# Kernel tuning notes

Hardware: AMD Instinct MI355X
Metric: run time of the kernel (lower is better)

The kernel has to match this reference:

```python
import jax, jax.numpy as jnp
import numpy as np

R, F, H = 256, 1024, 256  # num_robots, num_frontiers, hidden_dim


def setup_inputs() -> dict:
    key = jax.random.key(0)
    ks = jax.random.split(key, 16)
    sc = 0.05
    return {
        "robot_features": jax.random.normal(ks[0], (R, 4), jnp.float32),
        "frontier_features": jax.random.normal(ks[1], (F, 3), jnp.float32),
        # robot encoder: Linear(4,H) -> ReLU -> Linear(H,H)
        "r_w1": jax.random.normal(ks[2], (4, H), jnp.float32) * sc,
        "r_b1": jnp.zeros((H,), jnp.float32),
        "r_w2": jax.random.normal(ks[3], (H, H), jnp.float32) * sc,
        "r_b2": jnp.zeros((H,), jnp.float32),
        # frontier encoder: Linear(3,H) -> ReLU -> Linear(H,H)
        "f_w1": jax.random.normal(ks[4], (3, H), jnp.float32) * sc,
        "f_b1": jnp.zeros((H,), jnp.float32),
        "f_w2": jax.random.normal(ks[5], (H, H), jnp.float32) * sc,
        "f_b2": jnp.zeros((H,), jnp.float32),
        # affinity predictor: Linear(2H,H) -> ReLU -> Linear(H,1)
        "a_w1": jax.random.normal(ks[6], (2 * H, H), jnp.float32) * sc,
        "a_b1": jnp.zeros((H,), jnp.float32),
        "a_w2": jax.random.normal(ks[7], (H, 1), jnp.float32) * sc,
        "a_b2": jnp.zeros((1,), jnp.float32),
    }


def reference(robot_features, frontier_features,
              r_w1, r_b1, r_w2, r_b2,
              f_w1, f_b1, f_w2, f_b2,
              a_w1, a_b1, a_w2, a_b2):
    # encoders: Linear -> ReLU -> Linear
    robot_embed = jax.nn.relu(robot_features @ r_w1 + r_b1) @ r_w2 + r_b2      # (R, H)
    frontier_embed = jax.nn.relu(frontier_features @ f_w1 + f_b1) @ f_w2 + f_b2  # (F, H)

    # Vectorized pairwise concat: split a_w1 into robot/frontier halves so we
    # never materialize the (R, F, 2H) concat explicitly.
    w1_r, w1_f = a_w1[:robot_embed.shape[1]], a_w1[robot_embed.shape[1]:]
    h = robot_embed @ w1_r  # (R, H)
    h = h[:, None, :] + (frontier_embed @ w1_f)[None, :, :] + a_b1  # (R, F, H)
    h = jax.nn.relu(h)
    affinity = (h @ a_w2)[..., 0] + a_b2[0]  # (R, F)
    return affinity
```

## Files before the change

### kernel.cpp

```cpp
#include <hip/hip_runtime.h>
#include <hip/hip_bf16.h>

#define H 256
#define R_N 256
#define F_N 1024

#define FMA4(A, s, W) \
    A.x = fmaf((s), (W).x, A.x); \
    A.y = fmaf((s), (W).y, A.y); \
    A.z = fmaf((s), (W).z, A.z); \
    A.w = fmaf((s), (W).w, A.w);

__global__ __launch_bounds__(256) void embed_kernel(
    const float* __restrict__ rf, const float* __restrict__ ff,
    const float* __restrict__ r_w1, const float* __restrict__ r_b1,
    const float* __restrict__ r_w2, const float* __restrict__ r_b2,
    const float* __restrict__ f_w1, const float* __restrict__ f_b1,
    const float* __restrict__ f_w2, const float* __restrict__ f_b2,
    const float* __restrict__ a_w1, const float* __restrict__ a_b1,
    float* __restrict__ u, float* __restrict__ v)
{
    const int t  = threadIdx.x;
    const int wp = t >> 6;
    const int c  = (t & 63) * 4;

    __shared__ float aT[H][4];
    __shared__ float red[4][4][H];

    const bool robot = blockIdx.x < 64;
    const int  g0    = robot ? blockIdx.x * 4 : (blockIdx.x - 64) * 4;

    const float* __restrict__ x   = robot ? (rf + g0 * 4) : (ff + g0 * 3);
    const int                 ind = robot ? 4 : 3;
    const float* __restrict__ w1  = robot ? r_w1 : f_w1;
    const float* __restrict__ b1  = robot ? r_b1 : f_b1;
    const float* __restrict__ W2  = robot ? r_w2 : f_w2;
    const float* __restrict__ b2  = robot ? r_b2 : f_b2;
    const int                 k3  = robot ? 0 : H;
    float* __restrict__       dst = robot ? u : v;

    {
        float l1[4];
        const float bb = b1[t];
        #pragma unroll
        for (int g = 0; g < 4; ++g) {
            float acc = bb;
            for (int j = 0; j < ind; ++j)
                acc = fmaf(x[g * ind + j], w1[j * H + t], acc);
            l1[g] = fmaxf(acc, 0.0f);
        }
        *(float4*)&aT[t][0] = make_float4(l1[0], l1[1], l1[2], l1[3]);
    }
    __syncthreads();

    {
        float4 a0 = {0,0,0,0}, a1 = {0,0,0,0}, a2 = {0,0,0,0}, a3 = {0,0,0,0};
        const int kb = wp * 64;
        #pragma unroll 8
        for (int kk = 0; kk < 64; ++kk) {
            const int k = kb + kk;
            const float4 w4 = *(const float4*)&W2[k * H + c];
            const float4 av = *(const float4*)&aT[k][0];
            FMA4(a0, av.x, w4);
            FMA4(a1, av.y, w4);
            FMA4(a2, av.z, w4);
            FMA4(a3, av.w, w4);
        }
        *(float4*)&red[wp][0][c] = a0;
        *(float4*)&red[wp][1][c] = a1;
        *(float4*)&red[wp][2][c] = a2;
        *(float4*)&red[wp][3][c] = a3;
    }
    __syncthreads();

    {
        const float bb = b2[t];
        float e[4];
        #pragma unroll
        for (int g = 0; g < 4; ++g)
            e[g] = red[0][g][t] + red[1][g][t] + red[2][g][t] + red[3][g][t] + bb;
        __syncthreads();
        *(float4*)&aT[t][0] = make_float4(e[0], e[1], e[2], e[3]);
    }
    __syncthreads();

    {
        float4 a0 = {0,0,0,0}, a1 = {0,0,0,0}, a2 = {0,0,0,0}, a3 = {0,0,0,0};
        const int kb = wp * 64;
        #pragma unroll 8
        for (int kk = 0; kk < 64; ++kk) {
            const int k = kb + kk;
            const float4 w4 = *(const float4*)&a_w1[(k3 + k) * H + c];
            const float4 av = *(const float4*)&aT[k][0];
            FMA4(a0, av.x, w4);
            FMA4(a1, av.y, w4);
            FMA4(a2, av.z, w4);
            FMA4(a3, av.w, w4);
        }
        *(float4*)&red[wp][0][c] = a0;
        *(float4*)&red[wp][1][c] = a1;
        *(float4*)&red[wp][2][c] = a2;
        *(float4*)&red[wp][3][c] = a3;
    }
    __syncthreads();

    {
        const float ab = robot ? 0.0f : a_b1[t];
        #pragma unroll
        for (int g = 0; g < 4; ++g) {
            const float s = red[0][g][t] + red[1][g][t] + red[2][g][t] + red[3][g][t] + ab;
            dst[(g0 + g) * H + t] = s;
        }
    }
}

#define LDP 260

__global__ __launch_bounds__(512) void affinity_kernel(
    const float* __restrict__ u, const float* __restrict__ v,
    const float* __restrict__ a_w2, const float* __restrict__ a_b2,
    float* __restrict__ out)
{
    __shared__ float u_s[32][LDP];
    __shared__ float v_s[32][LDP];
    __shared__ float w_s[H];
    __shared__ float red[4][32][33];

    const int t  = threadIdx.x;
    const int r0 = (blockIdx.x >> 5) * 32;
    const int f0 = (blockIdx.x & 31) * 32;

    #pragma unroll
    for (int i = 0; i < 4; ++i) {
        const int slot = t + i * 512;
        const int row  = slot >> 6;
        const int cc   = (slot & 63) * 4;
        *(float4*)&u_s[row][cc] = *(const float4*)&u[(r0 + row) * H + cc];
        *(float4*)&v_s[row][cc] = *(const float4*)&v[(f0 + row) * H + cc];
    }
    if (t < 64) *(float4*)&w_s[t * 4] = *(const float4*)&a_w2[t * 4];
    __syncthreads();

    const int kp = t >> 7;
    const int t7 = t & 127;
    const int ri = t7 >> 4;
    const int fi = t7 & 15;
    const int k0 = kp * 64;

    float4 accA = make_float4(0.f, 0.f, 0.f, 0.f);
    float4 accB = make_float4(0.f, 0.f, 0.f, 0.f);

    #pragma unroll 4
    for (int kk = 0; kk < 64; kk += 4) {
        const int k = k0 + kk;
        const float4 w4 = *(const float4*)&w_s[k];
        const float4 u0 = *(const float4*)&u_s[ri][k];
        const float4 u1 = *(const float4*)&u_s[ri +  8][k];
        const float4 u2 = *(const float4*)&u_s[ri + 16][k];
        const float4 u3 = *(const float4*)&u_s[ri + 24][k];
        const float4 va = *(const float4*)&v_s[fi][k];
        const float4 vb = *(const float4*)&v_s[fi + 16][k];

        accA.x = fmaf(fmaxf(u0.x + va.x, 0.f), w4.x, accA.x);
        accA.x = fmaf(fmaxf(u0.y + va.y, 0.f), w4.y, accA.x);
        accA.x = fmaf(fmaxf(u0.z + va.z, 0.f), w4.z, accA.x);
        accA.x = fmaf(fmaxf(u0.w + va.w, 0.f), w4.w, accA.x);
        accA.y = fmaf(fmaxf(u1.x + va.x, 0.f), w4.x, accA.y);
        accA.y = fmaf(fmaxf(u1.y + va.y, 0.f), w4.y, accA.y);
        accA.y = fmaf(fmaxf(u1.z + va.z, 0.f), w4.z, accA.y);
        accA.y = fmaf(fmaxf(u1.w + va.w, 0.f), w4.w, accA.y);
        accA.z = fmaf(fmaxf(u2.x + va.x, 0.f), w4.x, accA.z);
        accA.z = fmaf(fmaxf(u2.y + va.y, 0.f), w4.y, accA.z);
        accA.z = fmaf(fmaxf(u2.z + va.z, 0.f), w4.z, accA.z);
        accA.z = fmaf(fmaxf(u2.w + va.w, 0.f), w4.w, accA.z);
        accA.w = fmaf(fmaxf(u3.x + va.x, 0.f), w4.x, accA.w);
        accA.w = fmaf(fmaxf(u3.y + va.y, 0.f), w4.y, accA.w);
        accA.w = fmaf(fmaxf(u3.z + va.z, 0.f), w4.z, accA.w);
        accA.w = fmaf(fmaxf(u3.w + va.w, 0.f), w4.w, accA.w);

        accB.x = fmaf(fmaxf(u0.x + vb.x, 0.f), w4.x, accB.x);
        accB.x = fmaf(fmaxf(u0.y + vb.y, 0.f), w4.y, accB.x);
        accB.x = fmaf(fmaxf(u0.z + vb.z, 0.f), w4.z, accB.x);
        accB.x = fmaf(fmaxf(u0.w + vb.w, 0.f), w4.w, accB.x);
        accB.y = fmaf(fmaxf(u1.x + vb.x, 0.f), w4.x, accB.y);
        accB.y = fmaf(fmaxf(u1.y + vb.y, 0.f), w4.y, accB.y);
        accB.y = fmaf(fmaxf(u1.z + vb.z, 0.f), w4.z, accB.y);
        accB.y = fmaf(fmaxf(u1.w + vb.w, 0.f), w4.w, accB.y);
        accB.z = fmaf(fmaxf(u2.x + vb.x, 0.f), w4.x, accB.z);
        accB.z = fmaf(fmaxf(u2.y + vb.y, 0.f), w4.y, accB.z);
        accB.z = fmaf(fmaxf(u2.z + vb.z, 0.f), w4.z, accB.z);
        accB.z = fmaf(fmaxf(u2.w + vb.w, 0.f), w4.w, accB.z);
        accB.w = fmaf(fmaxf(u3.x + vb.x, 0.f), w4.x, accB.w);
        accB.w = fmaf(fmaxf(u3.y + vb.y, 0.f), w4.y, accB.w);
        accB.w = fmaf(fmaxf(u3.z + vb.z, 0.f), w4.z, accB.w);
        accB.w = fmaf(fmaxf(u3.w + vb.w, 0.f), w4.w, accB.w);
    }

    red[kp][ri]     [fi]      = accA.x;
    red[kp][ri +  8][fi]      = accA.y;
    red[kp][ri + 16][fi]      = accA.z;
    red[kp][ri + 24][fi]      = accA.w;
    red[kp][ri]     [fi + 16] = accB.x;
    red[kp][ri +  8][fi + 16] = accB.y;
    red[kp][ri + 16][fi + 16] = accB.z;
    red[kp][ri + 24][fi + 16] = accB.w;
    __syncthreads();

    const float b = a_b2[0];
    #pragma unroll
    for (int j = 0; j < 2; ++j) {
        const int o = t + j * 512;
        const int r = o >> 5;
        const int f = o & 31;
        const float s = red[0][r][f] + red[1][r][f] + red[2][r][f] + red[3][r][f] + b;
        out[(r0 + r) * F_N + f0 + f] = s;
    }
}

extern "C" void kernel_launch(void* const* d_in, const int* in_sizes, int n_in,
                              void* d_out, int out_size, void* d_ws, size_t ws_size,
                              hipStream_t stream) {
    const float* rf   = (const float*)d_in[0];
    const float* ff   = (const float*)d_in[1];
    const float* r_w1 = (const float*)d_in[2];
    const float* r_b1 = (const float*)d_in[3];
    const float* r_w2 = (const float*)d_in[4];
    const float* r_b2 = (const float*)d_in[5];
    const float* f_w1 = (const float*)d_in[6];
    const float* f_b1 = (const float*)d_in[7];
    const float* f_w2 = (const float*)d_in[8];
    const float* f_b2 = (const float*)d_in[9];
    const float* a_w1 = (const float*)d_in[10];
    const float* a_b1 = (const float*)d_in[11];
    const float* a_w2 = (const float*)d_in[12];
    const float* a_b2 = (const float*)d_in[13];

    float* u = (float*)d_ws;
    float* v = u + R_N * H;

    embed_kernel<<<320, 256, 0, stream>>>(rf, ff, r_w1, r_b1, r_w2, r_b2,
                                          f_w1, f_b1, f_w2, f_b2,
                                          a_w1, a_b1, u, v);
    affinity_kernel<<<256, 512, 0, stream>>>(u, v, a_w2, a_b2, (float*)d_out);
}
```

Baseline: 26.11 us.

## Use 4x4 register tile per thread with 8-way K split in affinity kernel

Re-partitions the affinity kernel's thread work from a 4x2 (robot x frontier) output tile over a 4-way K split to a 4x4 tile over an 8-way K split of 32 columns each. Each thread loads 8 float4 rows from shared memory and reuses them for 16 accumulators instead of 6 loads for 8, cutting LDS traffic per FMA. In exchange the reduction buffer doubles to 8 partial slices and the final sum reads 8 values per output, adding shared memory and register pressure.

```diff
diff --git a/kernel.cpp b/kernel.cpp
--- a/kernel.cpp
+++ b/kernel.cpp
@@ -124,7 +124,7 @@
     __shared__ float u_s[32][LDP];
     __shared__ float v_s[32][LDP];
     __shared__ float w_s[H];
-    __shared__ float red[4][32][33];
+    __shared__ float red[8][32][33];
 
     const int t  = threadIdx.x;
     const int r0 = (blockIdx.x >> 5) * 32;
@@ -141,78 +141,58 @@
     if (t < 64) *(float4*)&w_s[t * 4] = *(const float4*)&a_w2[t * 4];
     __syncthreads();
 
-    const int kp = t >> 7;
-    const int t7 = t & 127;
-    const int ri = t7 >> 4;
-    const int fi = t7 & 15;
-    const int k0 = kp * 64;
-
-    float4 accA = make_float4(0.f, 0.f, 0.f, 0.f);
-    float4 accB = make_float4(0.f, 0.f, 0.f, 0.f);
+    const int kp = t >> 6;
+    const int t6 = t & 63;
+    const int ri = t6 & 7;
+    const int fi = t6 >> 3;
+    const int k0 = kp * 32;
+
+    float acc[4][4];
+    #pragma unroll
+    for (int a = 0; a < 4; ++a)
+        #pragma unroll
+        for (int b = 0; b < 4; ++b) acc[a][b] = 0.0f;
 
     #pragma unroll 4
-    for (int kk = 0; kk < 64; kk += 4) {
+    for (int kk = 0; kk < 32; kk += 4) {
         const int k = k0 + kk;
         const float4 w4 = *(const float4*)&w_s[k];
-        const float4 u0 = *(const float4*)&u_s[ri][k];
-        const float4 u1 = *(const float4*)&u_s[ri +  8][k];
-        const float4 u2 = *(const float4*)&u_s[ri + 16][k];
-        const float4 u3 = *(const float4*)&u_s[ri + 24][k];
-        const float4 va = *(const float4*)&v_s[fi][k];
-        const float4 vb = *(const float4*)&v_s[fi + 16][k];
-
-        accA.x = fmaf(fmaxf(u0.x + va.x, 0.f), w4.x, accA.x);
-        accA.x = fmaf(fmaxf(u0.y + va.y, 0.f), w4.y, accA.x);
-        accA.x = fmaf(fmaxf(u0.z + va.z, 0.f), w4.z, accA.x);
-        accA.x = fmaf(fmaxf(u0.w + va.w, 0.f), w4.w, accA.x);
-        accA.y = fmaf(fmaxf(u1.x + va.x, 0.f), w4.x, accA.y);
-        accA.y = fmaf(fmaxf(u1.y + va.y, 0.f), w4.y, accA.y);
-        accA.y = fmaf(fmaxf(u1.z + va.z, 0.f), w4.z, accA.y);
-        accA.y = fmaf(fmaxf(u1.w + va.w, 0.f), w4.w, accA.y);
-        accA.z = fmaf(fmaxf(u2.x + va.x, 0.f), w4.x, accA.z);
-        accA.z = fmaf(fmaxf(u2.y + va.y, 0.f), w4.y, accA.z);
-        accA.z = fmaf(fmaxf(u2.z + va.z, 0.f), w4.z, accA.z);
-        accA.z = fmaf(fmaxf(u2.w + va.w, 0.f), w4.w, accA.z);
-        accA.w = fmaf(fmaxf(u3.x + va.x, 0.f), w4.x, accA.w);
-        accA.w = fmaf(fmaxf(u3.y + va.y, 0.f), w4.y, accA.w);
-        accA.w = fmaf(fmaxf(u3.z + va.z, 0.f), w4.z, accA.w);
-        accA.w = fmaf(fmaxf(u3.w + va.w, 0.f), w4.w, accA.w);
-
-        accB.x = fmaf(fmaxf(u0.x + vb.x, 0.f), w4.x, accB.x);
-        accB.x = fmaf(fmaxf(u0.y + vb.y, 0.f), w4.y, accB.x);
-        accB.x = fmaf(fmaxf(u0.z + vb.z, 0.f), w4.z, accB.x);
-        accB.x = fmaf(fmaxf(u0.w + vb.w, 0.f), w4.w, accB.x);
-        accB.y = fmaf(fmaxf(u1.x + vb.x, 0.f), w4.x, accB.y);
-        accB.y = fmaf(fmaxf(u1.y + vb.y, 0.f), w4.y, accB.y);
-        accB.y = fmaf(fmaxf(u1.z + vb.z, 0.f), w4.z, accB.y);
-        accB.y = fmaf(fmaxf(u1.w + vb.w, 0.f), w4.w, accB.y);
-        accB.z = fmaf(fmaxf(u2.x + vb.x, 0.f), w4.x, accB.z);
-        accB.z = fmaf(fmaxf(u2.y + vb.y, 0.f), w4.y, accB.z);
-        accB.z = fmaf(fmaxf(u2.z + vb.z, 0.f), w4.z, accB.z);
-        accB.z = fmaf(fmaxf(u2.w + vb.w, 0.f), w4.w, accB.z);
-        accB.w = fmaf(fmaxf(u3.x + vb.x, 0.f), w4.x, accB.w);
-        accB.w = fmaf(fmaxf(u3.y + vb.y, 0.f), w4.y, accB.w);
-        accB.w = fmaf(fmaxf(u3.z + vb.z, 0.f), w4.z, accB.w);
-        accB.w = fmaf(fmaxf(u3.w + vb.w, 0.f), w4.w, accB.w);
-    }
-
-    red[kp][ri]     [fi]      = accA.x;
-    red[kp][ri +  8][fi]      = accA.y;
-    red[kp][ri + 16][fi]      = accA.z;
-    red[kp][ri + 24][fi]      = accA.w;
-    red[kp][ri]     [fi + 16] = accB.x;
-    red[kp][ri +  8][fi + 16] = accB.y;
-    red[kp][ri + 16][fi + 16] = accB.z;
-    red[kp][ri + 24][fi + 16] = accB.w;
-    __syncthreads();
-
-    const float b = a_b2[0];
+        float4 uu[4], vv[4];
+        #pragma unroll
+        for (int a = 0; a < 4; ++a) uu[a] = *(const float4*)&u_s[ri + 8 * a][k];
+        #pragma unroll
+        for (int b = 0; b < 4; ++b) vv[b] = *(const float4*)&v_s[fi + 8 * b][k];
+
+        #pragma unroll
+        for (int a = 0; a < 4; ++a) {
+            #pragma unroll
+            for (int b = 0; b < 4; ++b) {
+                float s = acc[a][b];
+                s = fmaf(fmaxf(uu[a].x + vv[b].x, 0.f), w4.x, s);
+                s = fmaf(fmaxf(uu[a].y + vv[b].y, 0.f), w4.y, s);
+                s = fmaf(fmaxf(uu[a].z + vv[b].z, 0.f), w4.z, s);
+                s = fmaf(fmaxf(uu[a].w + vv[b].w, 0.f), w4.w, s);
+                acc[a][b] = s;
+            }
+        }
+    }
+
+    #pragma unroll
+    for (int a = 0; a < 4; ++a)
+        #pragma unroll
+        for (int b = 0; b < 4; ++b)
+            red[kp][ri + 8 * a][fi + 8 * b] = acc[a][b];
+    __syncthreads();
+
+    const float bb = a_b2[0];
     #pragma unroll
     for (int j = 0; j < 2; ++j) {
         const int o = t + j * 512;
         const int r = o >> 5;
         const int f = o & 31;
-        const float s = red[0][r][f] + red[1][r][f] + red[2][r][f] + red[3][r][f] + b;
+        float s = bb;
+        #pragma unroll
+        for (int q = 0; q < 8; ++q) s += red[q][r][f];
         out[(r0 + r) * F_N + f0 + f] = s;
     }
 }
```

Measured after the change: 26.01 us. Within noise of the previous version (-0.4%).
